# Kernel tuning notes

Hardware: AMD Instinct MI355X
Metric: run time of the kernel (lower is better)

Reference implementation:

```python
import jax, jax.numpy as jnp
import numpy as np

WBITS = 2   # weight quantization bits (q_min_bits)
ABITS = 2   # activation quantization bits (out_bits, learnable since <=2)
SHIFT = 0   # activation pre-shift (config shift)


def quant_weight(w, bits=WBITS):
    """Symmetric per-tensor fake-quant with straight-through estimator."""
    qmax = 2.0 ** (bits - 1) - 1.0
    s = jnp.maximum(jnp.max(jnp.abs(w)) / qmax, 1e-8)
    q = jnp.round(w / s) * s
    return w + jax.lax.stop_gradient(q - w)


def quant_act(x, alpha, bits=ABITS, shift=SHIFT):
    """PACT-style learnable-clip activation fake-quant (unsigned, STE round)."""
    x = x * (2.0 ** (-shift))
    y = jnp.clip(x, 0.0, alpha)          # grad flows to alpha where clipped
    scale = alpha / (2.0 ** bits - 1.0)
    q = jnp.round(y / scale) * scale
    return y + jax.lax.stop_gradient(q - y)


def conv(x, w, pad):
    return jax.lax.conv_general_dilated(
        x, w, window_strides=(1, 1), padding=[(pad, pad), (pad, pad)],
        dimension_numbers=("NCHW", "OIHW", "NCHW"))


def maxpool2(x):
    return jax.lax.reduce_window(x, -jnp.inf, jax.lax.max,
                                 (1, 1, 2, 2), (1, 1, 2, 2), "VALID")


def setup_inputs() -> dict:
    key = jax.random.key(0)
    ks = jax.random.split(key, 5)
    B, H, W = 32, 224, 224
    x = jax.random.normal(ks[0], (B, 3, H, W), dtype=jnp.float32)
    # bits<=2 init branch: normal(mean=0, std=0.01)
    w1 = 0.01 * jax.random.normal(ks[1], (32, 3, 3, 3), dtype=jnp.float32)
    w2 = 0.01 * jax.random.normal(ks[2], (64, 32, 3, 3), dtype=jnp.float32)
    w3 = 0.01 * jax.random.normal(ks[3], (128, 64, 3, 3), dtype=jnp.float32)
    wc = 0.01 * jax.random.normal(ks[4], (10, 128, 1, 1), dtype=jnp.float32)
    a1 = jnp.ones((1,), jnp.float32)
    a2 = jnp.ones((1,), jnp.float32)
    a3 = jnp.ones((1,), jnp.float32)
    return {"x": x, "w1": w1, "w2": w2, "w3": w3, "wc": wc,
            "a1": a1, "a2": a2, "a3": a3}


def reference(x, w1, w2, w3, wc, a1, a2, a3):
    # block 1: QuantConv2d -> QuantizeActivation -> MaxPool2d(2)
    h = maxpool2(quant_act(conv(x, quant_weight(w1), 1), a1))
    # block 2
    h = maxpool2(quant_act(conv(h, quant_weight(w2), 1), a2))
    # block 3
    h = maxpool2(quant_act(conv(h, quant_weight(w3), 1), a3))
    # global amax pool over H, W (keepdim)
    h = jnp.max(h, axis=(2, 3), keepdims=True)
    # classifier: Dropout2d(eval=identity) + 1x1 QuantConv2d, no bias
    h = conv(h, quant_weight(wc), 0)
    return h.reshape(h.shape[0], -1)  # [B, num_classes]
```

## Files before the change

### kernel.cpp

```cpp
#include <hip/hip_runtime.h>
#include <math.h>


__global__ __launch_bounds__(256)
void prep_zero(unsigned* __restrict__ maxb, float* __restrict__ g) {
    const int i = blockIdx.x * 256 + threadIdx.x;
    if (i < 4) maxb[i] = 0u;
    if (i < 4096) g[i] = 0.f;
}

__global__ __launch_bounds__(256)
void prep_absmax(const float* __restrict__ w1, const float* __restrict__ w2,
                 const float* __restrict__ w3, const float* __restrict__ wc,
                 unsigned* __restrict__ maxb) {
    const float* srcs[4] = {w1, w2, w3, wc};
    const int    ns[4]   = {32*3*9, 64*32*9, 128*64*9, 10*128};
    const int t = blockIdx.y;
    const float* s = srcs[t];
    const int    N = ns[t];
    float m = 0.f;
    for (int i = blockIdx.x * 256 + threadIdx.x; i < N; i += 16 * 256)
        m = fmaxf(m, fabsf(s[i]));
    #pragma unroll
    for (int o = 32; o > 0; o >>= 1) m = fmaxf(m, __shfl_down(m, o));
    __shared__ float red[4];
    const int lane = threadIdx.x & 63, wid = threadIdx.x >> 6;
    if (lane == 0) red[wid] = m;
    __syncthreads();
    if (threadIdx.x == 0) {
        float mm = fmaxf(fmaxf(red[0], red[1]), fmaxf(red[2], red[3]));
        atomicMax(maxb + t, __float_as_uint(mm));
    }
}

__global__ __launch_bounds__(256)
void prep_qwc(const float* __restrict__ wc, const unsigned* __restrict__ maxb,
              float* __restrict__ qwc) {
    const float sc = fmaxf(__uint_as_float(maxb[3]), 1e-8f);
    const int i = blockIdx.x * 256 + threadIdx.x;
    if (i < 1280) qwc[i] = rintf(wc[i] / sc) * sc;
}

__global__ __launch_bounds__(256)
void build_lists(const float* __restrict__ w1, const float* __restrict__ w2,
                 const float* __restrict__ w3, const unsigned* __restrict__ maxb,
                 unsigned* __restrict__ h1, unsigned short* __restrict__ p1,
                 unsigned* __restrict__ h2, unsigned short* __restrict__ p2,
                 unsigned* __restrict__ h3, unsigned short* __restrict__ p3) {
    const float* wsrc[3] = {w1, w2, w3};
    unsigned*       hs[3] = {h1, h2, h3};
    unsigned short* ps[3] = {p1, p2, p3};
    const int cins[3] = {3, 32, 64};
    const int nch[3]  = {1, 8, 16};
    const int ngc[3]  = {2, 32, 128};
    const int t = blockIdx.y;
    const float* w = wsrc[t];
    const int CIN = cins[t], NCHUNK = nch[t];
    const int total = ngc[t] * 16;
    const float sc = fmaxf(__uint_as_float(maxb[t]), 1e-8f);
    for (int u = blockIdx.x * 256 + threadIdx.x; u < total; u += 8 * 256) {
        const int c = u & 15, rc = u >> 4;
        const int ch = rc % NCHUNK, grp = rc / NCHUNK;
        const int co = grp * 16 + c;
        unsigned* hdr = hs[t] + (size_t)rc * 36;
        unsigned short* inl = (unsigned short*)(hdr + 4);
        unsigned short* ovf = ps[t] + ((size_t)rc * 16 + c) * 32;
        int j = 0;
        for (int cil = 0; cil < 4; ++cil) {
            const int ci = ch * 4 + cil;
            if (ci >= CIN) break;
            for (int k = 0; k < 9; ++k) {
                const float q = rintf(w[(co * CIN + ci) * 9 + k] / sc);
                unsigned sgn;
                if (q > 0.5f)       sgn = 0u;
                else if (q < -0.5f) sgn = 0x8000u;
                else continue;
                const unsigned off = (unsigned)(cil * 1156 + (k / 3) * 34 + (k % 3));
                const unsigned short e = (unsigned short)(sgn | off);
                if (j < 4) inl[c * 4 + j] = e;
                else       ovf[j - 4] = e;
                ++j;
            }
        }
        ((unsigned char*)hdr)[c] = (unsigned char)j;
    }
}

template<int CIN, int Co, int LIDX>
__global__ __launch_bounds__(256, 4)
void conv_sparse(const float* __restrict__ in, const unsigned* __restrict__ hdrs,
                 const unsigned short* __restrict__ pool,
                 const unsigned* __restrict__ maxb,
                 const float* __restrict__ alpha_p, float* __restrict__ out,
                 int H, int W) {
    constexpr int NCHUNK = (CIN + 3) / 4;
    constexpr int CCH    = (CIN < 4) ? CIN : 4;
    constexpr int NGRP   = Co / 16;
    const int PH = H >> 1, PW = W >> 1;
    const int tx = threadIdx.x, ty = threadIdx.y;
    const int tid = ty * 16 + tx;
    const int b   = blockIdx.z / NGRP;
    const int grp = blockIdx.z % NGRP;
    const int px  = blockIdx.x * 16 + tx;
    const int py  = blockIdx.y * 16 + ty;
    const int ix0 = blockIdx.x * 32 - 1;
    const int iy0 = blockIdx.y * 32 - 1;

    __shared__ float tile[CCH * 1156];
    const size_t HW = (size_t)H * W;
    const float* inB = in + (size_t)b * CIN * HW;

    int sidx[5];
    #pragma unroll
    for (int s = 0; s < 5; ++s) {
        const int idx = tid + 256 * s;
        const int r = idx / 34, c = idx - r * 34;
        const int gy = iy0 + r, gx = ix0 + c;
        sidx[s] = (idx < 1156 && gy >= 0 && gy < H && gx >= 0 && gx < W)
                  ? (gy * W + gx) : -1;
    }

    float v[CCH][5];
    auto load_chunk = [&](int ch0) {
        #pragma unroll
        for (int ch = 0; ch < CCH; ++ch) {
            const float* inC = inB + (size_t)(ch0 + ch) * HW;
            #pragma unroll
            for (int s = 0; s < 5; ++s)
                v[ch][s] = (sidx[s] >= 0) ? inC[sidx[s]] : 0.f;
        }
    };
    auto store_tile = [&]() {
        #pragma unroll
        for (int ch = 0; ch < CCH; ++ch)
            #pragma unroll
            for (int s = 0; s < 5; ++s) {
                const int idx = tid + 256 * s;
                if (s < 4 || idx < 1156) tile[ch * 1156 + idx] = v[ch][s];
            }
    };

    const float sAbs = fmaxf(__uint_as_float(maxb[LIDX]), 1e-8f);
    const float sPos = __uint_as_float(__builtin_amdgcn_readfirstlane(__float_as_uint(sAbs)));
    const float sNeg = __uint_as_float(__builtin_amdgcn_readfirstlane(__float_as_uint(-sAbs)));

    float acc[16][4];
    #pragma unroll
    for (int c = 0; c < 16; ++c)
        #pragma unroll
        for (int q = 0; q < 4; ++q) acc[c][q] = 0.f;

    const int base = (2 * ty) * 34 + 2 * tx;

    load_chunk(0);

    #pragma unroll 1
    for (int chunk = 0; chunk < NCHUNK; ++chunk) {
        const unsigned* hdr = hdrs + (size_t)(grp * NCHUNK + chunk) * 36;
        unsigned cntd[4];
        #pragma unroll
        for (int i = 0; i < 4; ++i) cntd[i] = hdr[i];
        unsigned ent[32];
        #pragma unroll
        for (int i = 0; i < 32; ++i) ent[i] = hdr[4 + i];

        __syncthreads();
        store_tile();
        if (chunk + 1 < NCHUNK) load_chunk((chunk + 1) * 4);
        __syncthreads();

        const float* tb = tile + base;

        #pragma unroll
        for (int c = 0; c < 16; ++c) {
            const unsigned cnt = (cntd[c >> 2] >> ((c & 3) * 8)) & 0xffu;
            if (!cnt) continue;
            #pragma unroll
            for (int j = 0; j < 4; ++j) {
                if ((int)cnt > j) {
                    const unsigned e = (ent[2 * c + (j >> 1)] >> ((j & 1) * 16)) & 0xffffu;
                    const float wv = (e & 0x8000u) ? sNeg : sPos;
                    const float* q = tb + (e & 0x7fffu);
                    acc[c][0] = fmaf(wv, q[0],  acc[c][0]);
                    acc[c][1] = fmaf(wv, q[1],  acc[c][1]);
                    acc[c][2] = fmaf(wv, q[34], acc[c][2]);
                    acc[c][3] = fmaf(wv, q[35], acc[c][3]);
                }
            }
            if (cnt > 4) {
                const unsigned short* pp =
                    pool + ((size_t)(grp * NCHUNK + chunk) * 16 + c) * 32;
                #pragma unroll 1
                for (int j = 4; j < (int)cnt; ++j) {
                    const unsigned e = pp[j - 4];
                    const float wv = (e & 0x8000u) ? sNeg : sPos;
                    const float* q = tb + (e & 0x7fffu);
                    acc[c][0] = fmaf(wv, q[0],  acc[c][0]);
                    acc[c][1] = fmaf(wv, q[1],  acc[c][1]);
                    acc[c][2] = fmaf(wv, q[34], acc[c][2]);
                    acc[c][3] = fmaf(wv, q[35], acc[c][3]);
                }
            }
        }
    }

    if constexpr (LIDX == 2) {
        const float alpha = *alpha_p;
        const float scale = alpha / 3.0f;
        const bool valid = (py < PH) && (px < PW);
        float mv[16];
        #pragma unroll
        for (int c = 0; c < 16; ++c) {
            const float m = fmaxf(fmaxf(acc[c][0], acc[c][1]),
                                  fmaxf(acc[c][2], acc[c][3]));
            const float y = fminf(fmaxf(m, 0.f), alpha);
            const float q = rintf(y / scale) * scale;
            mv[c] = valid ? q : 0.f;
        }
        #pragma unroll
        for (int c = 0; c < 16; ++c)
            #pragma unroll
            for (int o = 32; o > 0; o >>= 1)
                mv[c] = fmaxf(mv[c], __shfl_down(mv[c], o));
        __shared__ float red[4][16];
        const int lane = tid & 63, wv = tid >> 6;
        if (lane == 0) {
            #pragma unroll
            for (int c = 0; c < 16; ++c) red[wv][c] = mv[c];
        }
        __syncthreads();
        if (tid < 16) {
            const float r = fmaxf(fmaxf(red[0][tid], red[1][tid]),
                                  fmaxf(red[2][tid], red[3][tid]));
            atomicMax((unsigned*)(out + (size_t)b * 128 + grp * 16 + tid),
                      __float_as_uint(r));
        }
    } else if (py < PH && px < PW) {
        const float alpha = *alpha_p;
        const float scale = alpha / 3.0f;
        #pragma unroll
        for (int c = 0; c < 16; ++c) {
            const float m = fmaxf(fmaxf(acc[c][0], acc[c][1]),
                                  fmaxf(acc[c][2], acc[c][3]));
            const float y = fminf(fmaxf(m, 0.f), alpha);
            out[(((size_t)b * Co + grp * 16 + c) * PH + py) * PW + px] =
                rintf(y / scale) * scale;
        }
    }
}

__global__ __launch_bounds__(128)
void classify_kernel(const float* __restrict__ g, const float* __restrict__ qwc,
                     float* __restrict__ out) {
    const int b = blockIdx.x;
    __shared__ float gg[128];
    gg[threadIdx.x] = g[b * 128 + threadIdx.x];
    __syncthreads();
    if (threadIdx.x < 10) {
        float s = 0.f;
        for (int k = 0; k < 128; ++k) s += qwc[threadIdx.x * 128 + k] * gg[k];
        out[b * 10 + threadIdx.x] = s;
    }
}

extern "C" void kernel_launch(void* const* d_in, const int* in_sizes, int n_in,
                              void* d_out, int out_size, void* d_ws, size_t ws_size,
                              hipStream_t stream) {
    const float* x  = (const float*)d_in[0];
    const float* w1 = (const float*)d_in[1];
    const float* w2 = (const float*)d_in[2];
    const float* w3 = (const float*)d_in[3];
    const float* wc = (const float*)d_in[4];
    const float* a1 = (const float*)d_in[5];
    const float* a2 = (const float*)d_in[6];
    const float* a3 = (const float*)d_in[7];

    float* ws = (float*)d_ws;
    size_t o = 0;
    float*    qwc  = ws + o; o += 1280;
    unsigned* maxb = (unsigned*)(ws + o); o += 4;
    float*    g    = ws + o; o += 32 * 128;
    unsigned*       h1 = (unsigned*)(ws + o);       o += 2   * 36;
    unsigned short* p1 = (unsigned short*)(ws + o); o += 2   * 16 * 16;
    unsigned*       h2 = (unsigned*)(ws + o);       o += 32  * 36;
    unsigned short* p2 = (unsigned short*)(ws + o); o += 32  * 16 * 16;
    unsigned*       h3 = (unsigned*)(ws + o);       o += 128 * 36;
    unsigned short* p3 = (unsigned short*)(ws + o); o += 128 * 16 * 16;
    float* h1p = ws + o; o += (size_t)32 * 32 * 112 * 112;
    float* h2p = ws + o; o += (size_t)32 * 64 * 56 * 56;

    prep_zero<<<16, 256, 0, stream>>>(maxb, g);
    prep_absmax<<<dim3(16, 4), 256, 0, stream>>>(w1, w2, w3, wc, maxb);
    prep_qwc<<<5, 256, 0, stream>>>(wc, maxb, qwc);
    build_lists<<<dim3(8, 3), 256, 0, stream>>>(w1, w2, w3, maxb,
                                                h1, p1, h2, p2, h3, p3);

    conv_sparse<3, 32, 0><<<dim3(7, 7, 32 * 2), dim3(16, 16), 0, stream>>>(
        x, h1, p1, maxb, a1, h1p, 224, 224);
    conv_sparse<32, 64, 1><<<dim3(4, 4, 32 * 4), dim3(16, 16), 0, stream>>>(
        h1p, h2, p2, maxb, a2, h2p, 112, 112);
    conv_sparse<64, 128, 2><<<dim3(2, 2, 32 * 8), dim3(16, 16), 0, stream>>>(
        h2p, h3, p3, maxb, a3, g, 56, 56);

    classify_kernel<<<32, 128, 0, stream>>>(g, qwc, (float*)d_out);
}
```

Measured before the change: 250.1 us.

## Shrink output-channel group and input chunk for layers 2-3 to raise occupancy

Parameterizes the sparse conv kernel by output-channel group width and channels per input chunk. Layers 2 and 3 now use groups of 8 output channels and 2-channel chunks with launch bounds allowing 8 waves per SIMD, which doubles the grid and cuts accumulator registers and shared-memory tile size. The next-chunk prefetch now starts after the second barrier instead of between the two barriers. In exchange, each input tile is loaded from global memory twice as many times across groups, and each block does more chunk iterations and barriers.

```diff
diff --git a/kernel.cpp b/kernel.cpp
--- a/kernel.cpp
+++ b/kernel.cpp
@@ -51,23 +51,26 @@
     unsigned*       hs[3] = {h1, h2, h3};
     unsigned short* ps[3] = {p1, p2, p3};
     const int cins[3] = {3, 32, 64};
-    const int nch[3]  = {1, 8, 16};
-    const int ngc[3]  = {2, 32, 128};
+    const int cchs[3] = {3, 2, 2};
+    const int nch[3]  = {1, 16, 32};
+    const int gws[3]  = {16, 8, 8};
+    const int rcs[3]  = {2, 128, 512};
     const int t = blockIdx.y;
     const float* w = wsrc[t];
-    const int CIN = cins[t], NCHUNK = nch[t];
-    const int total = ngc[t] * 16;
+    const int CIN = cins[t], CCH = cchs[t], NCHUNK = nch[t], GW = gws[t];
+    const int HDW = GW / 4 + 2 * GW;
+    const int total = rcs[t] * GW;
     const float sc = fmaxf(__uint_as_float(maxb[t]), 1e-8f);
     for (int u = blockIdx.x * 256 + threadIdx.x; u < total; u += 8 * 256) {
-        const int c = u & 15, rc = u >> 4;
+        const int c = u % GW, rc = u / GW;
         const int ch = rc % NCHUNK, grp = rc / NCHUNK;
-        const int co = grp * 16 + c;
-        unsigned* hdr = hs[t] + (size_t)rc * 36;
-        unsigned short* inl = (unsigned short*)(hdr + 4);
-        unsigned short* ovf = ps[t] + ((size_t)rc * 16 + c) * 32;
+        const int co = grp * GW + c;
+        unsigned* hdr = hs[t] + (size_t)rc * HDW;
+        unsigned short* inl = (unsigned short*)(hdr + GW / 4);
+        unsigned short* ovf = ps[t] + ((size_t)rc * GW + c) * 32;
         int j = 0;
-        for (int cil = 0; cil < 4; ++cil) {
-            const int ci = ch * 4 + cil;
+        for (int cil = 0; cil < CCH; ++cil) {
+            const int ci = ch * CCH + cil;
             if (ci >= CIN) break;
             for (int k = 0; k < 9; ++k) {
                 const float q = rintf(w[(co * CIN + ci) * 9 + k] / sc);
@@ -86,16 +89,17 @@
     }
 }
 
-template<int CIN, int Co, int LIDX>
-__global__ __launch_bounds__(256, 4)
+template<int CIN, int Co, int LIDX, int GW, int CCHp, int MINW>
+__global__ __launch_bounds__(256, MINW)
 void conv_sparse(const float* __restrict__ in, const unsigned* __restrict__ hdrs,
                  const unsigned short* __restrict__ pool,
                  const unsigned* __restrict__ maxb,
                  const float* __restrict__ alpha_p, float* __restrict__ out,
                  int H, int W) {
-    constexpr int NCHUNK = (CIN + 3) / 4;
-    constexpr int CCH    = (CIN < 4) ? CIN : 4;
-    constexpr int NGRP   = Co / 16;
+    constexpr int CCH    = (CIN < CCHp) ? CIN : CCHp;
+    constexpr int NCHUNK = (CIN + CCH - 1) / CCH;
+    constexpr int NGRP   = Co / GW;
+    constexpr int HDW    = GW / 4 + 2 * GW;
     const int PH = H >> 1, PW = W >> 1;
     const int tx = threadIdx.x, ty = threadIdx.y;
     const int tid = ty * 16 + tx;
@@ -144,9 +148,9 @@
     const float sPos = __uint_as_float(__builtin_amdgcn_readfirstlane(__float_as_uint(sAbs)));
     const float sNeg = __uint_as_float(__builtin_amdgcn_readfirstlane(__float_as_uint(-sAbs)));
 
-    float acc[16][4];
+    float acc[GW][4];
     #pragma unroll
-    for (int c = 0; c < 16; ++c)
+    for (int c = 0; c < GW; ++c)
         #pragma unroll
         for (int q = 0; q < 4; ++q) acc[c][q] = 0.f;
 
@@ -156,23 +160,23 @@
 
     #pragma unroll 1
     for (int chunk = 0; chunk < NCHUNK; ++chunk) {
-        const unsigned* hdr = hdrs + (size_t)(grp * NCHUNK + chunk) * 36;
-        unsigned cntd[4];
-        #pragma unroll
-        for (int i = 0; i < 4; ++i) cntd[i] = hdr[i];
-        unsigned ent[32];
-        #pragma unroll
-        for (int i = 0; i < 32; ++i) ent[i] = hdr[4 + i];
+        const unsigned* hdr = hdrs + (size_t)(grp * NCHUNK + chunk) * HDW;
+        unsigned cntd[GW / 4];
+        #pragma unroll
+        for (int i = 0; i < GW / 4; ++i) cntd[i] = hdr[i];
+        unsigned ent[2 * GW];
+        #pragma unroll
+        for (int i = 0; i < 2 * GW; ++i) ent[i] = hdr[GW / 4 + i];
 
         __syncthreads();
         store_tile();
-        if (chunk + 1 < NCHUNK) load_chunk((chunk + 1) * 4);
         __syncthreads();
+        if (chunk + 1 < NCHUNK) load_chunk((chunk + 1) * CCH);
 
         const float* tb = tile + base;
 
         #pragma unroll
-        for (int c = 0; c < 16; ++c) {
+        for (int c = 0; c < GW; ++c) {
             const unsigned cnt = (cntd[c >> 2] >> ((c & 3) * 8)) & 0xffu;
             if (!cnt) continue;
             #pragma unroll
@@ -189,7 +193,7 @@
             }
             if (cnt > 4) {
                 const unsigned short* pp =
-                    pool + ((size_t)(grp * NCHUNK + chunk) * 16 + c) * 32;
+                    pool + ((size_t)(grp * NCHUNK + chunk) * GW + c) * 32;
                 #pragma unroll 1
                 for (int j = 4; j < (int)cnt; ++j) {
                     const unsigned e = pp[j - 4];
@@ -208,9 +212,9 @@
         const float alpha = *alpha_p;
         const float scale = alpha / 3.0f;
         const bool valid = (py < PH) && (px < PW);
-        float mv[16];
-        #pragma unroll
-        for (int c = 0; c < 16; ++c) {
+        float mv[GW];
+        #pragma unroll
+        for (int c = 0; c < GW; ++c) {
             const float m = fmaxf(fmaxf(acc[c][0], acc[c][1]),
                                   fmaxf(acc[c][2], acc[c][3]));
             const float y = fminf(fmaxf(m, 0.f), alpha);
@@ -218,32 +222,32 @@
             mv[c] = valid ? q : 0.f;
         }
         #pragma unroll
-        for (int c = 0; c < 16; ++c)
+        for (int c = 0; c < GW; ++c)
             #pragma unroll
             for (int o = 32; o > 0; o >>= 1)
                 mv[c] = fmaxf(mv[c], __shfl_down(mv[c], o));
-        __shared__ float red[4][16];
+        __shared__ float red[4][GW];
         const int lane = tid & 63, wv = tid >> 6;
         if (lane == 0) {
             #pragma unroll
-            for (int c = 0; c < 16; ++c) red[wv][c] = mv[c];
+            for (int c = 0; c < GW; ++c) red[wv][c] = mv[c];
         }
         __syncthreads();
-        if (tid < 16) {
+        if (tid < GW) {
             const float r = fmaxf(fmaxf(red[0][tid], red[1][tid]),
                                   fmaxf(red[2][tid], red[3][tid]));
-            atomicMax((unsigned*)(out + (size_t)b * 128 + grp * 16 + tid),
+            atomicMax((unsigned*)(out + (size_t)b * 128 + grp * GW + tid),
                       __float_as_uint(r));
         }
     } else if (py < PH && px < PW) {
         const float alpha = *alpha_p;
         const float scale = alpha / 3.0f;
         #pragma unroll
-        for (int c = 0; c < 16; ++c) {
+        for (int c = 0; c < GW; ++c) {
             const float m = fmaxf(fmaxf(acc[c][0], acc[c][1]),
                                   fmaxf(acc[c][2], acc[c][3]));
             const float y = fminf(fmaxf(m, 0.f), alpha);
-            out[(((size_t)b * Co + grp * 16 + c) * PH + py) * PW + px] =
+            out[(((size_t)b * Co + grp * GW + c) * PH + py) * PW + px] =
                 rintf(y / scale) * scale;
         }
     }
@@ -281,11 +285,11 @@
     unsigned* maxb = (unsigned*)(ws + o); o += 4;
     float*    g    = ws + o; o += 32 * 128;
     unsigned*       h1 = (unsigned*)(ws + o);       o += 2   * 36;
-    unsigned short* p1 = (unsigned short*)(ws + o); o += 2   * 16 * 16;
-    unsigned*       h2 = (unsigned*)(ws + o);       o += 32  * 36;
-    unsigned short* p2 = (unsigned short*)(ws + o); o += 32  * 16 * 16;
-    unsigned*       h3 = (unsigned*)(ws + o);       o += 128 * 36;
-    unsigned short* p3 = (unsigned short*)(ws + o); o += 128 * 16 * 16;
+    unsigned short* p1 = (unsigned short*)(ws + o); o += 512;
+    unsigned*       h2 = (unsigned*)(ws + o);       o += 128 * 18;
+    unsigned short* p2 = (unsigned short*)(ws + o); o += 16384;
+    unsigned*       h3 = (unsigned*)(ws + o);       o += 512 * 18;
+    unsigned short* p3 = (unsigned short*)(ws + o); o += 65536;
     float* h1p = ws + o; o += (size_t)32 * 32 * 112 * 112;
     float* h2p = ws + o; o += (size_t)32 * 64 * 56 * 56;
 
@@ -295,11 +299,11 @@
     build_lists<<<dim3(8, 3), 256, 0, stream>>>(w1, w2, w3, maxb,
                                                 h1, p1, h2, p2, h3, p3);
 
-    conv_sparse<3, 32, 0><<<dim3(7, 7, 32 * 2), dim3(16, 16), 0, stream>>>(
+    conv_sparse<3, 32, 0, 16, 3, 4><<<dim3(7, 7, 32 * 2), dim3(16, 16), 0, stream>>>(
         x, h1, p1, maxb, a1, h1p, 224, 224);
-    conv_sparse<32, 64, 1><<<dim3(4, 4, 32 * 4), dim3(16, 16), 0, stream>>>(
+    conv_sparse<32, 64, 1, 8, 2, 8><<<dim3(4, 4, 32 * 8), dim3(16, 16), 0, stream>>>(
         h1p, h2, p2, maxb, a2, h2p, 112, 112);
-    conv_sparse<64, 128, 2><<<dim3(2, 2, 32 * 8), dim3(16, 16), 0, stream>>>(
+    conv_sparse<64, 128, 2, 8, 2, 8><<<dim3(2, 2, 32 * 16), dim3(16, 16), 0, stream>>>(
         h2p, h3, p3, maxb, a3, g, 56, 56);
 
     classify_kernel<<<32, 128, 0, stream>>>(g, qwc, (float*)d_out);
```

Measured after the change: 266.3 us. 6.5% more time.
